# Performance work log

Measured on AMD Instinct MI355X. Metric: run time of the kernel, lower is better.

Reference implementation:

```python
import jax, jax.numpy as jnp
import numpy as np

N_QUBITS = 4
N_LAYERS = 2


def _apply_1q_shared(state, gate, wire):
    # state: [N,2,2,2,2] (axis wire+1 = qubit 'wire'), gate: [2,2] complex
    st = jnp.moveaxis(state, wire + 1, -1)
    st = jnp.einsum('ij,nabcj->nabci', gate, st)
    return jnp.moveaxis(st, -1, wire + 1)


def _apply_1q_batched(state, gate, wire):
    # gate: [N,2,2] (per-sample angles)
    st = jnp.moveaxis(state, wire + 1, -1)
    st = jnp.einsum('nij,nabcj->nabci', gate, st)
    return jnp.moveaxis(st, -1, wire + 1)


def _cnot(state, c, t):
    s0 = jnp.take(state, 0, axis=c + 1)
    s1 = jnp.take(state, 1, axis=c + 1)
    t_ax = t if t > c else t + 1  # target axis after removing control axis
    s1 = jnp.flip(s1, axis=t_ax)
    return jnp.stack([s0, s1], axis=c + 1)


def _ry_mat_batched(theta):
    c = jnp.cos(theta / 2).astype(jnp.complex64)
    s = jnp.sin(theta / 2).astype(jnp.complex64)
    return jnp.stack([jnp.stack([c, -s], -1), jnp.stack([s, c], -1)], -2)


def _rx_mat(theta):
    c = jnp.cos(theta / 2).astype(jnp.complex64)
    s = (-1j * jnp.sin(theta / 2)).astype(jnp.complex64)
    return jnp.array(0).astype(jnp.complex64) + jnp.stack([jnp.stack([c, s]), jnp.stack([s, c])])


def _ry_mat(theta):
    c = jnp.cos(theta / 2).astype(jnp.complex64)
    s = jnp.sin(theta / 2).astype(jnp.complex64)
    return jnp.stack([jnp.stack([c, -s]), jnp.stack([s, c])])


def _rz_mat(theta):
    e = jnp.exp(-0.5j * theta.astype(jnp.complex64))
    z = jnp.zeros((), jnp.complex64)
    return jnp.stack([jnp.stack([e, z]), jnp.stack([z, jnp.conj(e)])])


def setup_inputs() -> dict:
    key = jax.random.key(0)
    k1, k2 = jax.random.split(key)
    x = jax.random.normal(k1, (32, 3, 128, 128), dtype=jnp.float32)
    weights = 0.1 * jax.random.normal(k2, (N_LAYERS, N_QUBITS, 3), dtype=jnp.float32)
    return {'x': x, 'weights': weights}


def reference(x, weights):
    B, C, H, W = x.shape
    # 2x2 patches, stride 1, flattened row-major: [N,4]
    patches = jnp.stack(
        [x[:, :, :-1, :-1], x[:, :, :-1, 1:], x[:, :, 1:, :-1], x[:, :, 1:, 1:]],
        axis=-1,
    ).reshape(-1, 4)
    N = patches.shape[0]

    # |0000> state, axis layout [N, q0, q1, q2, q3] (wire 0 most significant)
    state = jnp.zeros((N, 2, 2, 2, 2), jnp.complex64).at[:, 0, 0, 0, 0].set(1.0)

    # RY data encoding (per-patch angles)
    for q in range(N_QUBITS):
        state = _apply_1q_batched(state, _ry_mat_batched(patches[:, q]), q)

    for layer in range(N_LAYERS):
        for q in range(N_QUBITS):
            state = _apply_1q_shared(state, _rx_mat(weights[layer, q, 0]), q)
            state = _apply_1q_shared(state, _ry_mat(weights[layer, q, 1]), q)
            state = _apply_1q_shared(state, _rz_mat(weights[layer, q, 2]), q)
        state = _cnot(state, 0, 1)
        state = _cnot(state, 2, 3)
        state = _cnot(state, 0, 2)
        state = _cnot(state, 1, 3)

    probs = jnp.abs(state) ** 2  # [N,2,2,2,2] real
    ev = probs[:, 0].sum(axis=(1, 2, 3)) - probs[:, 1].sum(axis=(1, 2, 3))  # <Z0>
    return ev.reshape(B, C, H - 1, W - 1).astype(x.dtype)
```

## Files before the change

kernel.cpp:

```cpp
#include <hip/hip_runtime.h>
#include <hip/hip_bf16.h>


using f32x2 = __attribute__((ext_vector_type(2))) float;

__device__ __forceinline__ void compute_W_block(const float* __restrict__ wts,
                                                float* __restrict__ Wsh,
                                                int simw) {
    __shared__ float2 U[16][16];
    __shared__ float  A[16][16];
    const int tid  = threadIdx.x;
    const int wave = tid >> 6;
    const int lane = tid & 63;

    if (wave == simw && lane < 16) {
        const int col = lane;
        float2 v[16];
        #pragma unroll
        for (int i = 0; i < 16; ++i) v[i] = make_float2(i == col ? 1.f : 0.f, 0.f);

        #pragma unroll
        for (int layer = 0; layer < 2; ++layer) {
            #pragma unroll
            for (int q = 0; q < 4; ++q) {
                const int p = 3 - q;
                const float thx = wts[(layer * 4 + q) * 3 + 0];
                const float thy = wts[(layer * 4 + q) * 3 + 1];
                const float thz = wts[(layer * 4 + q) * 3 + 2];
                {
                    float c = __cosf(0.5f * thx), s = __sinf(0.5f * thx);
                    #pragma unroll
                    for (int i = 0; i < 16; ++i) if (!((i >> p) & 1)) {
                        const int j = i | (1 << p);
                        float2 a = v[i], b = v[j];
                        v[i] = make_float2(c * a.x + s * b.y, c * a.y - s * b.x);
                        v[j] = make_float2(c * b.x + s * a.y, c * b.y - s * a.x);
                    }
                }
                {
                    float c = __cosf(0.5f * thy), s = __sinf(0.5f * thy);
                    #pragma unroll
                    for (int i = 0; i < 16; ++i) if (!((i >> p) & 1)) {
                        const int j = i | (1 << p);
                        float2 a = v[i], b = v[j];
                        v[i] = make_float2(c * a.x - s * b.x, c * a.y - s * b.y);
                        v[j] = make_float2(s * a.x + c * b.x, s * a.y + c * b.y);
                    }
                }
                {
                    float c = __cosf(0.5f * thz), s = __sinf(0.5f * thz);
                    #pragma unroll
                    for (int i = 0; i < 16; ++i) {
                        float2 a = v[i];
                        if (!((i >> p) & 1)) v[i] = make_float2(c * a.x + s * a.y, c * a.y - s * a.x);
                        else                 v[i] = make_float2(c * a.x - s * a.y, c * a.y + s * a.x);
                    }
                }
            }
            #pragma unroll
            for (int ee = 0; ee < 4; ++ee) {
                const int cc[4] = {0, 2, 0, 1}, tt[4] = {1, 3, 2, 3};
                const int pc = 3 - cc[ee], pt = 3 - tt[ee];
                #pragma unroll
                for (int i = 0; i < 16; ++i) if (((i >> pc) & 1) && !((i >> pt) & 1)) {
                    const int j = i | (1 << pt);
                    float2 t = v[i]; v[i] = v[j]; v[j] = t;
                }
            }
        }
        #pragma unroll
        for (int i = 0; i < 16; ++i) U[col][i] = v[i];
    }
    __syncthreads();

    {
        const int j = tid >> 4, k = tid & 15;
        float re = 0.f;
        #pragma unroll
        for (int i = 0; i < 16; ++i) {
            const float z = (i & 8) ? -1.f : 1.f;
            float2 a = U[j][i], b = U[k][i];
            re += z * (a.x * b.x + a.y * b.y);
        }
        A[j][k] = re;
    }
    __syncthreads();

    if (tid < 84) {
        float r = 0.f;
        if (tid < 81) {
            const int e = tid;
            const int d0 = e / 27, d1 = (e / 9) % 3, d2 = (e / 3) % 3, d3 = e % 3;
            int mask1 = 0, mask2 = 0;
            if (d0 == 1) mask1 |= 8; else if (d0 == 2) mask2 |= 8;
            if (d1 == 1) mask1 |= 4; else if (d1 == 2) mask2 |= 4;
            if (d2 == 1) mask1 |= 2; else if (d2 == 2) mask2 |= 2;
            if (d3 == 1) mask1 |= 1; else if (d3 == 2) mask2 |= 1;
            float sum = 0.f;
            #pragma unroll
            for (int b = 0; b < 16; ++b) {
                const float sgn = (__popc(b & mask1) & 1) ? -1.f : 1.f;
                sum += sgn * A[b][b ^ mask2];
            }
            r = sum * 0.0625f;
        }
        Wsh[tid] = r;
    }
    __syncthreads();
}

__global__ __launch_bounds__(256, 4) void qconv_fused(
        const float* __restrict__ x, const float* __restrict__ wts,
        float* __restrict__ out) {
    __shared__ __align__(16) float Wsh[84];

    const int g    = blockIdx.x * 8 + (threadIdx.x >> 5);
    const int l    = threadIdx.x & 31;
    const int img  = g >> 6;
    const int pair = g & 63;
    const int h    = pair * 2;
    const int nr   = (pair == 63) ? 1 : 2;
    const int col0 = l * 4;
    const int ncols = (l == 31) ? 3 : 4;
    const int base = img * 16384 + h * 128 + col0;

    float r0[5], r1[5], r2[5];
    {
        float4 a4 = *(const float4*)(x + base);
        float4 b4 = *(const float4*)(x + base + 128);
        r0[0]=a4.x; r0[1]=a4.y; r0[2]=a4.z; r0[3]=a4.w;
        r1[0]=b4.x; r1[1]=b4.y; r1[2]=b4.z; r1[3]=b4.w;
        r0[4]=0.f; r1[4]=0.f; r2[0]=0.f; r2[1]=0.f; r2[2]=0.f; r2[3]=0.f; r2[4]=0.f;
        if (ncols == 4) { r0[4] = x[base + 4]; r1[4] = x[base + 132]; }
        if (nr == 2) {
            float4 c4 = *(const float4*)(x + base + 256);
            r2[0]=c4.x; r2[1]=c4.y; r2[2]=c4.z; r2[3]=c4.w;
            if (ncols == 4) r2[4] = x[base + 260];
        }
    }

    f32x2 ctv[5], stv[5], cbv[5], sbv[5];
    #pragma unroll
    for (int j = 0; j < 5; ++j) {
        float s0 = __sinf(r0[j]), c0 = __cosf(r0[j]);
        float s1 = __sinf(r1[j]), c1 = __cosf(r1[j]);
        float s2 = __sinf(r2[j]), c2 = __cosf(r2[j]);
        ctv[j] = (f32x2){c0, c1};  stv[j] = (f32x2){s0, s1};
        cbv[j] = (f32x2){c1, c2};  sbv[j] = (f32x2){s1, s2};
    }

    compute_W_block(wts, Wsh, blockIdx.x & 3);

    f32x2 acc[4];
    #pragma unroll
    for (int k = 0; k < 4; ++k) acc[k] = (f32x2){0.f, 0.f};

    #pragma unroll
    for (int e0 = 0; e0 < 3; ++e0) {
        f32x2 a0[4];
        #pragma unroll
        for (int k = 0; k < 4; ++k) a0[k] = (f32x2){0.f, 0.f};
        #pragma unroll
        for (int e1 = 0; e1 < 3; ++e1) {
            f32x2 a1[4];
            #pragma unroll
            for (int k = 0; k < 4; ++k) a1[k] = (f32x2){0.f, 0.f};
            #pragma unroll
            for (int e2 = 0; e2 < 3; ++e2) {
                const int idx = ((e0 * 3 + e1) * 3 + e2) * 3;
                const float w0 = Wsh[idx], w1 = Wsh[idx + 1], w2 = Wsh[idx + 2];
                #pragma unroll
                for (int k = 0; k < 4; ++k) {
                    f32x2 a2 = w0 + w1 * cbv[k + 1] + w2 * sbv[k + 1];
                    if (e2 == 0)      a1[k] += a2;
                    else if (e2 == 1) a1[k] += a2 * cbv[k];
                    else              a1[k] += a2 * sbv[k];
                }
            }
            #pragma unroll
            for (int k = 0; k < 4; ++k) {
                if (e1 == 0)      a0[k] += a1[k];
                else if (e1 == 1) a0[k] += a1[k] * ctv[k + 1];
                else              a0[k] += a1[k] * stv[k + 1];
            }
        }
        #pragma unroll
        for (int k = 0; k < 4; ++k) {
            if (e0 == 0)      acc[k] += a0[k];
            else if (e0 == 1) acc[k] += a0[k] * ctv[k];
            else              acc[k] += a0[k] * stv[k];
        }
    }

    const int ob0 = (img * 127 + h) * 127 + col0;
    #pragma unroll
    for (int k = 0; k < 4; ++k) if (k < ncols) out[ob0 + k] = acc[k].x;
    if (nr == 2) {
        const int ob1 = ob0 + 127;
        #pragma unroll
        for (int k = 0; k < 4; ++k) if (k < ncols) out[ob1 + k] = acc[k].y;
    }
}

extern "C" void kernel_launch(void* const* d_in, const int* in_sizes, int n_in,
                              void* d_out, int out_size, void* d_ws, size_t ws_size,
                              hipStream_t stream) {
    const float* x   = (const float*)d_in[0];
    const float* wts = (const float*)d_in[1];
    float* out = (float*)d_out;

    const int blocks = (96 * 64) / 8;
    qconv_fused<<<blocks, 256, 0, stream>>>(x, wts, out);
}
```

Before: 14.70 us.

## Split weight-tensor precompute into a separate single-block setup kernel

The 81-coefficient transfer tensor was previously rebuilt in every block, costing a serial 16-lane circuit simulation plus two syncs per block. It is now computed once by a single-block setup kernel into workspace, and the main kernel only loads 81 floats into shared memory. This adds a second kernel launch and a dependency between the two, whose launch and serialization overhead may offset the per-block savings at this small kernel time.

```diff
diff --git a/kernel.cpp b/kernel.cpp
--- a/kernel.cpp
+++ b/kernel.cpp
@@ -4,20 +4,15 @@
 
 using f32x2 = __attribute__((ext_vector_type(2))) float;
 
-__device__ __forceinline__ void compute_W_block(const float* __restrict__ wts,
-                                                float* __restrict__ Wsh,
-                                                int simw) {
+__global__ void qconv_setup(const float* __restrict__ wts, float* __restrict__ W) {
     __shared__ float2 U[16][16];
     __shared__ float  A[16][16];
-    const int tid  = threadIdx.x;
-    const int wave = tid >> 6;
-    const int lane = tid & 63;
-
-    if (wave == simw && lane < 16) {
-        const int col = lane;
+    const int tid = threadIdx.x;
+
+    if (tid < 16) {
         float2 v[16];
         #pragma unroll
-        for (int i = 0; i < 16; ++i) v[i] = make_float2(i == col ? 1.f : 0.f, 0.f);
+        for (int i = 0; i < 16; ++i) v[i] = make_float2(i == tid ? 1.f : 0.f, 0.f);
 
         #pragma unroll
         for (int layer = 0; layer < 2; ++layer) {
@@ -69,7 +64,7 @@
             }
         }
         #pragma unroll
-        for (int i = 0; i < 16; ++i) U[col][i] = v[i];
+        for (int i = 0; i < 16; ++i) U[tid][i] = v[i];
     }
     __syncthreads();
 
@@ -86,33 +81,30 @@
     }
     __syncthreads();
 
-    if (tid < 84) {
-        float r = 0.f;
-        if (tid < 81) {
-            const int e = tid;
-            const int d0 = e / 27, d1 = (e / 9) % 3, d2 = (e / 3) % 3, d3 = e % 3;
-            int mask1 = 0, mask2 = 0;
-            if (d0 == 1) mask1 |= 8; else if (d0 == 2) mask2 |= 8;
-            if (d1 == 1) mask1 |= 4; else if (d1 == 2) mask2 |= 4;
-            if (d2 == 1) mask1 |= 2; else if (d2 == 2) mask2 |= 2;
-            if (d3 == 1) mask1 |= 1; else if (d3 == 2) mask2 |= 1;
-            float sum = 0.f;
-            #pragma unroll
-            for (int b = 0; b < 16; ++b) {
-                const float sgn = (__popc(b & mask1) & 1) ? -1.f : 1.f;
-                sum += sgn * A[b][b ^ mask2];
-            }
-            r = sum * 0.0625f;
-        }
-        Wsh[tid] = r;
-    }
-    __syncthreads();
+    if (tid < 81) {
+        const int e = tid;
+        const int d0 = e / 27, d1 = (e / 9) % 3, d2 = (e / 3) % 3, d3 = e % 3;
+        int mask1 = 0, mask2 = 0;
+        if (d0 == 1) mask1 |= 8; else if (d0 == 2) mask2 |= 8;
+        if (d1 == 1) mask1 |= 4; else if (d1 == 2) mask2 |= 4;
+        if (d2 == 1) mask1 |= 2; else if (d2 == 2) mask2 |= 2;
+        if (d3 == 1) mask1 |= 1; else if (d3 == 2) mask2 |= 1;
+        float sum = 0.f;
+        #pragma unroll
+        for (int b = 0; b < 16; ++b) {
+            const float sgn = (__popc(b & mask1) & 1) ? -1.f : 1.f;
+            sum += sgn * A[b][b ^ mask2];
+        }
+        W[e] = sum * 0.0625f;
+    }
 }
 
-__global__ __launch_bounds__(256, 4) void qconv_fused(
-        const float* __restrict__ x, const float* __restrict__ wts,
+__global__ __launch_bounds__(256, 4) void qconv_main(
+        const float* __restrict__ x, const float* __restrict__ Wg,
         float* __restrict__ out) {
-    __shared__ __align__(16) float Wsh[84];
+    __shared__ float Wsh[84];
+    if (threadIdx.x < 84)
+        Wsh[threadIdx.x] = (threadIdx.x < 81) ? Wg[threadIdx.x] : 0.f;
 
     const int g    = blockIdx.x * 8 + (threadIdx.x >> 5);
     const int l    = threadIdx.x & 31;
@@ -149,7 +141,7 @@
         cbv[j] = (f32x2){c1, c2};  sbv[j] = (f32x2){s1, s2};
     }
 
-    compute_W_block(wts, Wsh, blockIdx.x & 3);
+    __syncthreads();
 
     f32x2 acc[4];
     #pragma unroll
@@ -208,7 +200,10 @@
     const float* x   = (const float*)d_in[0];
     const float* wts = (const float*)d_in[1];
     float* out = (float*)d_out;
+    float* W   = (float*)d_ws;
+
+    qconv_setup<<<1, 256, 0, stream>>>(wts, W);
 
     const int blocks = (96 * 64) / 8;
-    qconv_fused<<<blocks, 256, 0, stream>>>(x, wts, out);
+    qconv_main<<<blocks, 256, 0, stream>>>(x, W, out);
 }
```

Result: slower. 16.52 us (+12.4%).
